# Performance work log

Measured on AMD Instinct MI355X. Metric: run time of the kernel, lower is better.

## Reference

```python
import jax, jax.numpy as jnp
import numpy as np

B, H, W, C = 8, 56, 56, 256
HEADS = 8      # block-level heads; each branch uses HEADS//2
SPLIT = 7      # split_size
EPS = 1e-5


def _ln(x, g, b):
    m = x.mean(-1, keepdims=True)
    v = ((x - m) ** 2).mean(-1, keepdims=True)
    return (x - m) * jax.lax.rsqrt(v + EPS) * g + b


def _lepe_attn(q, k, v, H_sp, W_sp, heads, cw, cb):
    # q,k,v: [B,H,W,Ch]; cross-shaped window attention with LePE depthwise conv bias
    Bq, Hq, Wq, Ch = q.shape
    hd = Ch // heads
    scale = hd ** -0.5
    nh, nw = Hq // H_sp, Wq // W_sp

    def win(t):  # -> [Bw, heads, L, hd]  (Bw = B*nh*nw, L = H_sp*W_sp)
        t = t.reshape(Bq, nh, H_sp, nw, W_sp, Ch).transpose(0, 1, 3, 2, 4, 5)
        return t.reshape(-1, H_sp * W_sp, heads, hd).transpose(0, 2, 1, 3)

    qw, kw = win(q), win(k)
    # v windows laid out NCHW for the depthwise LePE conv
    vimg = v.reshape(Bq, nh, H_sp, nw, W_sp, Ch).transpose(0, 1, 3, 5, 2, 4).reshape(-1, Ch, H_sp, W_sp)
    lepe = jax.lax.conv_general_dilated(
        vimg, cw, window_strides=(1, 1), padding=((1, 1), (1, 1)),
        feature_group_count=Ch, dimension_numbers=("NCHW", "OIHW", "NCHW"))
    lepe = lepe + cb[None, :, None, None]
    lepe = lepe.reshape(-1, heads, hd, H_sp * W_sp).transpose(0, 1, 3, 2)
    vw = vimg.reshape(-1, heads, hd, H_sp * W_sp).transpose(0, 1, 3, 2)

    attn = jax.nn.softmax(jnp.einsum("whld,whmd->whlm", qw * scale, kw), axis=-1)
    out = jnp.einsum("whlm,whmd->whld", attn, vw) + lepe  # [Bw,heads,L,hd]
    out = out.transpose(0, 2, 1, 3).reshape(-1, H_sp, W_sp, Ch)
    # windows2img
    out = out.reshape(Bq, nh, nw, H_sp, W_sp, Ch).transpose(0, 1, 3, 2, 4, 5).reshape(Bq, Hq, Wq, Ch)
    return out


def setup_inputs() -> dict:
    key = jax.random.key(0)
    ks = jax.random.split(key, 8)
    ch = C // 2
    s = 0.02
    return {
        "x": jax.random.normal(ks[0], (B, H, W, C), jnp.float32),
        "gamma1": jnp.ones((C,), jnp.float32), "beta1": jnp.zeros((C,), jnp.float32),
        "w_qkv": jax.random.normal(ks[1], (C, 3 * C), jnp.float32) * s,
        "lepe_w0": jax.random.normal(ks[2], (ch, 1, 3, 3), jnp.float32) * s,
        "lepe_b0": jnp.zeros((ch,), jnp.float32),
        "lepe_w1": jax.random.normal(ks[3], (ch, 1, 3, 3), jnp.float32) * s,
        "lepe_b1": jnp.zeros((ch,), jnp.float32),
        "w_proj": jax.random.normal(ks[4], (C, C), jnp.float32) * s,
        "b_proj": jnp.zeros((C,), jnp.float32),
        "gamma2": jnp.ones((C,), jnp.float32), "beta2": jnp.zeros((C,), jnp.float32),
        "w_fc1": jax.random.normal(ks[5], (C, 4 * C), jnp.float32) * s,
        "b_fc1": jnp.zeros((4 * C,), jnp.float32),
        "w_fc2": jax.random.normal(ks[6], (4 * C, C), jnp.float32) * s,
        "b_fc2": jnp.zeros((C,), jnp.float32),
    }


def reference(x, gamma1, beta1, w_qkv, lepe_w0, lepe_b0, lepe_w1, lepe_b1,
              w_proj, b_proj, gamma2, beta2, w_fc1, b_fc1, w_fc2, b_fc2):
    Bx, Hx, Wx, Cx = x.shape
    img = _ln(x, gamma1, beta1)
    qkv = (img @ w_qkv).reshape(Bx, Hx, Wx, 3, Cx).transpose(3, 0, 1, 2, 4)
    q, k, v = qkv[0], qkv[1], qkv[2]
    ch = Cx // 2
    heads = HEADS // 2
    # branch 0 (idx=0): H_sp=H, W_sp=split  -> vertical stripes
    x0 = _lepe_attn(q[..., :ch], k[..., :ch], v[..., :ch], Hx, SPLIT, heads, lepe_w0, lepe_b0)
    # branch 1 (idx=1): H_sp=split, W_sp=W  -> horizontal stripes
    x1 = _lepe_attn(q[..., ch:], k[..., ch:], v[..., ch:], SPLIT, Wx, heads, lepe_w1, lepe_b1)
    att = jnp.concatenate([x0, x1], axis=-1) @ w_proj + b_proj
    x = x + att
    h = _ln(x, gamma2, beta2)
    h = jax.nn.gelu(h @ w_fc1 + b_fc1, approximate=False) @ w_fc2 + b_fc2
    return x + h
```

## Files before the change

kernel.cpp:

```cpp
#include <hip/hip_runtime.h>
#include <stdint.h>

typedef __attribute__((ext_vector_type(4))) float  f32x4;
typedef __attribute__((ext_vector_type(8))) __bf16 bf16x8;

#define DEVI static __device__ __forceinline__

DEVI float bf2f_lo(uint32_t u) { union { uint32_t i; float f; } v; v.i = u << 16;          return v.f; }
DEVI float bf2f_hi(uint32_t u) { union { uint32_t i; float f; } v; v.i = u & 0xffff0000u;  return v.f; }
DEVI uint16_t f2bf(float f) {
    union { float f; uint32_t i; } v; v.f = f;
    uint32_t r = v.i + 0x7fffu + ((v.i >> 16) & 1u);
    return (uint16_t)(r >> 16);
}
DEVI void unpack8(uint4 u, float* f) {
    f[0] = bf2f_lo(u.x); f[1] = bf2f_hi(u.x);
    f[2] = bf2f_lo(u.y); f[3] = bf2f_hi(u.y);
    f[4] = bf2f_lo(u.z); f[5] = bf2f_hi(u.z);
    f[6] = bf2f_lo(u.w); f[7] = bf2f_hi(u.w);
}
DEVI void gload_lds16(const uint16_t* gp, uint16_t* lp) {
    __builtin_amdgcn_global_load_lds(
        (const __attribute__((address_space(1))) uint32_t*)gp,
        (__attribute__((address_space(3))) uint32_t*)lp, 16, 0, 0);
}

__global__ __launch_bounds__(256) void wprep(const float* __restrict__ w,
                                             uint16_t* __restrict__ wt, int K, int N) {
    int idx = blockIdx.x * 256 + threadIdx.x;
    if (idx >= K * N) return;
    int k = idx / N, n = idx - k * N;
    wt[(size_t)n * K + k] = f2bf(w[idx]);
}

__global__ __launch_bounds__(256) void ln_kernel(const float* __restrict__ x,
                                                 const float* __restrict__ g,
                                                 const float* __restrict__ be,
                                                 uint16_t* __restrict__ y) {
    int row  = blockIdx.x * 4 + (threadIdx.x >> 6);
    int lane = threadIdx.x & 63;
    const float* xr = x + (size_t)row * 256 + lane * 4;
    f32x4 v = *(const f32x4*)xr;
    float s  = v[0] + v[1] + v[2] + v[3];
    float s2 = v[0]*v[0] + v[1]*v[1] + v[2]*v[2] + v[3]*v[3];
#pragma unroll
    for (int off = 32; off > 0; off >>= 1) {
        s  += __shfl_xor(s, off);
        s2 += __shfl_xor(s2, off);
    }
    float mean = s * (1.f / 256.f);
    float var  = s2 * (1.f / 256.f) - mean * mean;
    float rs   = rsqrtf(var + 1e-5f);
    f32x4 gv = *(const f32x4*)(g  + lane * 4);
    f32x4 bv = *(const f32x4*)(be + lane * 4);
    uint64_t pk = 0;
#pragma unroll
    for (int j = 0; j < 4; ++j) {
        uint64_t b = f2bf((v[j] - mean) * rs * gv[j] + bv[j]);
        pk |= b << (16 * j);
    }
    *(uint64_t*)(y + (size_t)row * 256 + lane * 4) = pk;
}

template <int EPI>
__global__ __launch_bounds__(256) void gemm_bt(const uint16_t* __restrict__ A,
                                               const uint16_t* __restrict__ Bt,
                                               int M, int N, int K,
                                               const float* __restrict__ bias,
                                               const float* __restrict__ resid,
                                               void* __restrict__ outp) {
    __shared__ __align__(16) uint16_t As[2][128 * 32];
    __shared__ __align__(16) uint16_t Bs[2][128 * 32];
    const int tid  = threadIdx.x;
    const int lane = tid & 63;
    const int w    = tid >> 6;
    const int wr   = w >> 1, wc = w & 1;
    const int bm = blockIdx.x, bn = blockIdx.y;
    f32x4 acc[4][4] = {};
    const int nk = K >> 5;
    const int wb = w * 512;

    const int srow = tid >> 2;
    const int hwr  = (srow ^ (srow >> 2)) & 3;
    const size_t ao0 = (size_t)srow * K + (size_t)(((tid & 3) ^ hwr) * 8);
    const size_t ao1 = ao0 + (size_t)64 * K;

    const uint16_t* Abase = A  + (size_t)bm * 128 * K;
    const uint16_t* Bbase = Bt + (size_t)bn * 128 * K;

    auto stage = [&](int buf, int kk) {
        const uint16_t* Ab = Abase + kk * 32;
        const uint16_t* Bb = Bbase + kk * 32;
        gload_lds16(Ab + ao0, &As[buf][wb]);
        gload_lds16(Ab + ao1, &As[buf][wb + 2048]);
        gload_lds16(Bb + ao0, &Bs[buf][wb]);
        gload_lds16(Bb + ao1, &Bs[buf][wb + 2048]);
    };

    stage(0, 0);
    __syncthreads();
    int cur = 0;

    const int li = lane & 15;
    const int rA = wr * 64 + li;
    const int rB = wc * 64 + li;
    const int kx = ((lane >> 4) ^ ((li ^ (li >> 2)) & 3)) * 8;

    for (int kk = 0; kk < nk; ++kk) {
        if (kk + 1 < nk) stage(cur ^ 1, kk + 1);

        bf16x8 af[4], bfr[4];
#pragma unroll
        for (int m = 0; m < 4; ++m)
            af[m] = __builtin_bit_cast(bf16x8,
                     *(const uint4*)&As[cur][(rA + m * 16) * 32 + kx]);
#pragma unroll
        for (int n = 0; n < 4; ++n)
            bfr[n] = __builtin_bit_cast(bf16x8,
                      *(const uint4*)&Bs[cur][(rB + n * 16) * 32 + kx]);
#pragma unroll
        for (int m = 0; m < 4; ++m)
#pragma unroll
            for (int n = 0; n < 4; ++n)
                acc[m][n] = __builtin_amdgcn_mfma_f32_16x16x32_bf16(af[m], bfr[n], acc[m][n], 0, 0, 0);

        __syncthreads();
        cur ^= 1;
    }

    const int row0 = bm * 128 + wr * 64 + ((lane >> 4) * 4);
    const int col0 = bn * 128 + wc * 64 + li;
#pragma unroll
    for (int m = 0; m < 4; ++m) {
#pragma unroll
        for (int n = 0; n < 4; ++n) {
            const int col = col0 + n * 16;
#pragma unroll
            for (int r = 0; r < 4; ++r) {
                const int row = row0 + m * 16 + r;
                float v = acc[m][n][r];
                size_t idx = (size_t)row * N + col;
                if (EPI == 0) {
                    ((uint16_t*)outp)[idx] = f2bf(v);
                } else if (EPI == 1) {
                    ((float*)outp)[idx] = v + bias[col] + resid[idx];
                } else {
                    v += bias[col];
                    float ge = 0.5f * v * (1.0f + erff(v * 0.70710678118654752f));
                    ((uint16_t*)outp)[idx] = f2bf(ge);
                }
            }
        }
    }
}

__global__ __launch_bounds__(64) void attn_mfma(const uint16_t* __restrict__ qkv,
                                                uint16_t* __restrict__ att) {
    __shared__ __align__(16) uint16_t Pl[64 * 40];
    int bid = blockIdx.x;
    const int qtile = bid % 7;  bid /= 7;
    const int head  = bid & 3;  bid >>= 2;
    const int win   = bid & 63; bid >>= 6;
    const int branch = bid;
    const int lane = threadIdx.x;
    const int g  = lane >> 4;
    const int li = lane & 15;
    const int b = win >> 3, wp = win & 7;
    const int ch0 = branch * 128 + head * 32;
    const int base0 = b * 3136;
    const int woff  = wp * 7;
    const int toks1 = base0 + wp * 392;

    auto tokof = [&](int l) -> int {
        if (branch == 0) { int r = l / 7; return base0 + r * 56 + woff + (l - r * 7); }
        return toks1 + l;
    };
    const int tok391 = tokof(391);
    const int q0 = qtile * 64;

    bf16x8 qf[4];
#pragma unroll
    for (int nb = 0; nb < 4; ++nb) {
        int ql = q0 + nb * 16 + li; if (ql > 391) ql = 391;
        qf[nb] = __builtin_bit_cast(bf16x8,
                 *(const uint4*)(qkv + (size_t)tokof(ql) * 768 + ch0 + g * 8));
    }

    float m_run[4], s_run[4];
    f32x4 oacc[2][4];
#pragma unroll
    for (int nb = 0; nb < 4; ++nb) {
        m_run[nb] = -1e30f; s_run[nb] = 0.f;
        oacc[0][nb] = (f32x4)0.f; oacc[1][nb] = (f32x4)0.f;
    }
    const float scale = 0.17677669529663687f;

    for (int kt = 0; kt < 13; ++kt) {
        const int kbase = kt * 32;
        bf16x8 kf[2];
#pragma unroll
        for (int mb = 0; mb < 2; ++mb) {
            int kl = kbase + mb * 16 + li; if (kl > 391) kl = 391;
            kf[mb] = __builtin_bit_cast(bf16x8,
                     *(const uint4*)(qkv + (size_t)tokof(kl) * 768 + 256 + ch0 + g * 8));
        }
        uint16_t vg0[8], vg1[8];
        {
            int kl0 = kbase + g * 8;
            int tk, cc = 0;
            if (branch == 0) { int r = kl0 / 7; cc = kl0 - r * 7; tk = base0 + r * 56 + woff + cc; }
            else tk = toks1 + kl0;
#pragma unroll
            for (int j = 0; j < 8; ++j) {
                int t = (kl0 + j > 391) ? tok391 : tk;
                const uint16_t* vp = qkv + (size_t)t * 768 + 512 + ch0 + li;
                vg0[j] = vp[0];
                vg1[j] = vp[16];
                if (branch == 0) { if (++cc == 7) { cc = 0; tk += 50; } else ++tk; }
                else ++tk;
            }
        }
        f32x4 sa[2][4] = {};
#pragma unroll
        for (int mb = 0; mb < 2; ++mb)
#pragma unroll
            for (int nb = 0; nb < 4; ++nb)
                sa[mb][nb] = __builtin_amdgcn_mfma_f32_16x16x32_bf16(kf[mb], qf[nb], sa[mb][nb], 0, 0, 0);
#pragma unroll
        for (int mb = 0; mb < 2; ++mb)
#pragma unroll
            for (int nb = 0; nb < 4; ++nb)
#pragma unroll
                for (int r = 0; r < 4; ++r) sa[mb][nb][r] *= scale;
        if (kt == 12) {
#pragma unroll
            for (int nb = 0; nb < 4; ++nb)
#pragma unroll
                for (int r = 0; r < 4; ++r) {
                    if (g >= 2) sa[0][nb][r] = -1e30f;
                    sa[1][nb][r] = -1e30f;
                }
        }
#pragma unroll
        for (int nb = 0; nb < 4; ++nb) {
            f32x4 mx = sa[0][nb];
#pragma unroll
            for (int r = 0; r < 4; ++r) mx[r] = fmaxf(mx[r], sa[1][nb][r]);
            float mt = fmaxf(fmaxf(mx[0], mx[1]), fmaxf(mx[2], mx[3]));
            mt = fmaxf(mt, __shfl_xor(mt, 16));
            mt = fmaxf(mt, __shfl_xor(mt, 32));
            float m_new = fmaxf(m_run[nb], mt);
            float corr = __expf(m_run[nb] - m_new);
            m_run[nb] = m_new;
#pragma unroll
            for (int mb = 0; mb < 2; ++mb)
#pragma unroll
                for (int r = 0; r < 4; ++r) oacc[mb][nb][r] *= corr;
            float psum = 0.f;
            uint32_t pk[4];
#pragma unroll
            for (int mb = 0; mb < 2; ++mb) {
                float p0 = __expf(sa[mb][nb][0] - m_new);
                float p1 = __expf(sa[mb][nb][1] - m_new);
                float p2 = __expf(sa[mb][nb][2] - m_new);
                float p3 = __expf(sa[mb][nb][3] - m_new);
                psum += (p0 + p1) + (p2 + p3);
                pk[mb * 2 + 0] = (uint32_t)f2bf(p0) | ((uint32_t)f2bf(p1) << 16);
                pk[mb * 2 + 1] = (uint32_t)f2bf(p2) | ((uint32_t)f2bf(p3) << 16);
            }
            psum += __shfl_xor(psum, 16);
            psum += __shfl_xor(psum, 32);
            s_run[nb] = s_run[nb] * corr + psum;
            uint32_t* dst = (uint32_t*)&Pl[(li + 16 * nb) * 40];
            dst[g * 2 + 0] = pk[0];
            dst[g * 2 + 1] = pk[1];
            dst[g * 2 + 8] = pk[2];
            dst[g * 2 + 9] = pk[3];
        }
        union { uint16_t u[8]; bf16x8 v; } cv0, cv1;
#pragma unroll
        for (int j = 0; j < 8; ++j) { cv0.u[j] = vg0[j]; cv1.u[j] = vg1[j]; }
        bf16x8 vf0 = cv0.v, vf1 = cv1.v;
        bf16x8 pf[4];
#pragma unroll
        for (int nb = 0; nb < 4; ++nb)
            pf[nb] = __builtin_bit_cast(bf16x8,
                     *(const uint4*)&Pl[(li + 16 * nb) * 40 + g * 8]);
#pragma unroll
        for (int nb = 0; nb < 4; ++nb) {
            oacc[0][nb] = __builtin_amdgcn_mfma_f32_16x16x32_bf16(vf0, pf[nb], oacc[0][nb], 0, 0, 0);
            oacc[1][nb] = __builtin_amdgcn_mfma_f32_16x16x32_bf16(vf1, pf[nb], oacc[1][nb], 0, 0, 0);
        }
    }
#pragma unroll
    for (int nb = 0; nb < 4; ++nb) {
        int ql = q0 + nb * 16 + li;
        if (ql <= 391) {
            float rn = 1.f / s_run[nb];
            uint16_t* op = att + (size_t)tokof(ql) * 256 + ch0;
#pragma unroll
            for (int mb = 0; mb < 2; ++mb)
#pragma unroll
                for (int r = 0; r < 4; ++r)
                    op[mb * 16 + g * 4 + r] = f2bf(oacc[mb][nb][r] * rn);
        }
    }
}

__global__ __launch_bounds__(256) void lepe_kernel(const uint16_t* __restrict__ qkv,
                                                   const float* __restrict__ lw0,
                                                   const float* __restrict__ lb0,
                                                   const float* __restrict__ lw1,
                                                   const float* __restrict__ lb1,
                                                   uint16_t* __restrict__ att) {
    __shared__ float wl[9][256];
    __shared__ float bl[256];
    {
        int tid = threadIdx.x;
        for (int i = tid; i < 2304; i += 256) {
            int tap = i >> 8, ch = i & 255;
            wl[tap][ch] = (ch < 128) ? lw0[ch * 9 + tap] : lw1[(ch - 128) * 9 + tap];
        }
        bl[tid] = (tid < 128) ? lb0[tid] : lb1[tid - 128];
    }
    __syncthreads();

    int idx = blockIdx.x * 256 + threadIdx.x;
    int t = idx >> 5, cg = idx & 31;
    int ch = cg * 8;
    int branch = ch >> 7;
    int b = t / 3136, rem = t - b * 3136, h = rem / 56, w = rem - h * 56;
    int r0, r1, c0, c1;
    if (branch == 0) { r0 = 0; r1 = 55; int wp = w / 7; c0 = wp * 7; c1 = c0 + 6; }
    else             { int hp = h / 7; r0 = hp * 7; r1 = r0 + 6; c0 = 0; c1 = 55; }

    const uint16_t* vbase = qkv + (size_t)b * 3136 * 768 + 512 + ch;
    float acc[8];
    {
        f32x4 b0 = *(const f32x4*)&bl[ch];
        f32x4 b1 = *(const f32x4*)&bl[ch + 4];
#pragma unroll
        for (int d = 0; d < 4; ++d) { acc[d] = b0[d]; acc[d + 4] = b1[d]; }
    }
#pragma unroll
    for (int dy = -1; dy <= 1; ++dy) {
#pragma unroll
        for (int dx = -1; dx <= 1; ++dx) {
            int hh = h + dy, ww = w + dx;
            float mask = (hh >= r0 && hh <= r1 && ww >= c0 && ww <= c1) ? 1.f : 0.f;
            int hc = min(max(hh, r0), r1), wc = min(max(ww, c0), c1);
            uint4 u = *(const uint4*)(vbase + (size_t)(hc * 56 + wc) * 768);
            float vv[8]; unpack8(u, vv);
            const int tap = (dy + 1) * 3 + (dx + 1);
            f32x4 w0 = *(const f32x4*)&wl[tap][ch];
            f32x4 w1 = *(const f32x4*)&wl[tap][ch + 4];
#pragma unroll
            for (int d = 0; d < 4; ++d) {
                acc[d]     += (mask * w0[d]) * vv[d];
                acc[d + 4] += (mask * w1[d]) * vv[d + 4];
            }
        }
    }
    uint16_t* ap = att + (size_t)t * 256 + ch;
    uint4 a = *(const uint4*)ap;
    float av[8]; unpack8(a, av);
    uint16_t ob[8];
#pragma unroll
    for (int d = 0; d < 8; ++d) ob[d] = f2bf(av[d] + acc[d]);
    *(uint4*)ap = *(const uint4*)ob;
}

extern "C" void kernel_launch(void* const* d_in, const int* in_sizes, int n_in,
                              void* d_out, int out_size, void* d_ws, size_t ws_size,
                              hipStream_t stream) {
    const float* x      = (const float*)d_in[0];
    const float* g1     = (const float*)d_in[1];
    const float* be1    = (const float*)d_in[2];
    const float* w_qkv  = (const float*)d_in[3];
    const float* lw0    = (const float*)d_in[4];
    const float* lb0    = (const float*)d_in[5];
    const float* lw1    = (const float*)d_in[6];
    const float* lb1    = (const float*)d_in[7];
    const float* w_proj = (const float*)d_in[8];
    const float* b_proj = (const float*)d_in[9];
    const float* g2     = (const float*)d_in[10];
    const float* be2    = (const float*)d_in[11];
    const float* w_fc1  = (const float*)d_in[12];
    const float* b_fc1  = (const float*)d_in[13];
    const float* w_fc2  = (const float*)d_in[14];
    const float* b_fc2  = (const float*)d_in[15];
    float* out = (float*)d_out;

    char* p = (char*)d_ws;
    auto carve = [&](size_t bytes) -> char* {
        char* q = p; p += (bytes + 255) & ~(size_t)255; return q;
    };
    uint16_t* lnb    = (uint16_t*)carve((size_t)25088 * 256 * 2);
    uint16_t* qkvh   = (uint16_t*)carve((size_t)25088 * 1024 * 2);
    uint16_t* attb   = (uint16_t*)carve((size_t)25088 * 256 * 2);
    float*    x1     = (float*)   carve((size_t)25088 * 256 * 4);
    uint16_t* wqkvT  = (uint16_t*)carve((size_t)768 * 256 * 2);
    uint16_t* wprojT = (uint16_t*)carve((size_t)256 * 256 * 2);
    uint16_t* wfc1T  = (uint16_t*)carve((size_t)1024 * 256 * 2);
    uint16_t* wfc2T  = (uint16_t*)carve((size_t)256 * 1024 * 2);

    wprep<<<768,  256, 0, stream>>>(w_qkv,  wqkvT,  256, 768);
    wprep<<<256,  256, 0, stream>>>(w_proj, wprojT, 256, 256);
    wprep<<<1024, 256, 0, stream>>>(w_fc1,  wfc1T,  256, 1024);
    wprep<<<1024, 256, 0, stream>>>(w_fc2,  wfc2T,  1024, 256);

    ln_kernel<<<6272, 256, 0, stream>>>(x, g1, be1, lnb);
    gemm_bt<0><<<dim3(196, 6), 256, 0, stream>>>(lnb, wqkvT, 25088, 768, 256,
                                                 nullptr, nullptr, qkvh);
    attn_mfma<<<3584, 64, 0, stream>>>(qkvh, attb);
    lepe_kernel<<<3136, 256, 0, stream>>>(qkvh, lw0, lb0, lw1, lb1, attb);
    gemm_bt<1><<<dim3(196, 2), 256, 0, stream>>>(attb, wprojT, 25088, 256, 256,
                                                 b_proj, x, x1);
    ln_kernel<<<6272, 256, 0, stream>>>(x1, g2, be2, lnb);
    gemm_bt<2><<<dim3(196, 8), 256, 0, stream>>>(lnb, wfc1T, 25088, 1024, 256,
                                                 b_fc1, nullptr, qkvh);
    gemm_bt<1><<<dim3(196, 2), 256, 0, stream>>>(qkvh, wfc2T, 25088, 256, 1024,
                                                 b_fc2, x1, out);
}
```

Baseline: 310.2 us.

## Fold softmax scale into exp2, add lazy rescale, remap block order

The explicit multiply of the score tiles by the softmax scale is removed. The scale and log2(e) are folded into one constant used with exp2f and an fma. The running-max rescale of the accumulators now happens only when some lane's new max exceeds the old one by more than a threshold, which skips most of the correction multiplies. Block indices are permuted so that neighbouring workgroups land on different XCDs with a different grouping of window, head and tile, and the bf16 conversion uses the native cast. The lazy rescale lets exponentials grow up to 2^8 before correction, which is safe in fp32 but could in principle affect bf16 P precision.

```diff
diff --git a/kernel.cpp b/kernel.cpp
--- a/kernel.cpp
+++ b/kernel.cpp
@@ -157,11 +157,13 @@
 __global__ __launch_bounds__(64) void attn_mfma(const uint16_t* __restrict__ qkv,
                                                 uint16_t* __restrict__ att) {
     __shared__ __align__(16) uint16_t Pl[64 * 40];
-    int bid = blockIdx.x;
-    const int qtile = bid % 7;  bid /= 7;
-    const int head  = bid & 3;  bid >>= 2;
-    const int win   = bid & 63; bid >>= 6;
-    const int branch = bid;
+    int bid = ((int)blockIdx.x & 7) * 448 + ((int)blockIdx.x >> 3);
+    const int sub   = bid % 28;
+    const int winl  = bid / 28;
+    const int qtile = sub % 7;
+    const int head  = sub / 7;
+    const int win   = winl & 63;
+    const int branch = winl >> 6;
     const int lane = threadIdx.x;
     const int g  = lane >> 4;
     const int li = lane & 15;
@@ -193,7 +195,8 @@
         m_run[nb] = -1e30f; s_run[nb] = 0.f;
         oacc[0][nb] = (f32x4)0.f; oacc[1][nb] = (f32x4)0.f;
     }
-    const float scale = 0.17677669529663687f;
+    const float c = 0.25503486f;
+    const float THR = 31.368f;
 
     for (int kt = 0; kt < 13; ++kt) {
         const int kbase = kt * 32;
@@ -226,12 +229,6 @@
 #pragma unroll
             for (int nb = 0; nb < 4; ++nb)
                 sa[mb][nb] = __builtin_amdgcn_mfma_f32_16x16x32_bf16(kf[mb], qf[nb], sa[mb][nb], 0, 0, 0);
-#pragma unroll
-        for (int mb = 0; mb < 2; ++mb)
-#pragma unroll
-            for (int nb = 0; nb < 4; ++nb)
-#pragma unroll
-                for (int r = 0; r < 4; ++r) sa[mb][nb][r] *= scale;
         if (kt == 12) {
 #pragma unroll
             for (int nb = 0; nb < 4; ++nb)
@@ -243,34 +240,39 @@
         }
 #pragma unroll
         for (int nb = 0; nb < 4; ++nb) {
-            f32x4 mx = sa[0][nb];
-#pragma unroll
-            for (int r = 0; r < 4; ++r) mx[r] = fmaxf(mx[r], sa[1][nb][r]);
-            float mt = fmaxf(fmaxf(mx[0], mx[1]), fmaxf(mx[2], mx[3]));
+            float mt = fmaxf(fmaxf(fmaxf(sa[0][nb][0], sa[0][nb][1]), fmaxf(sa[0][nb][2], sa[0][nb][3])),
+                             fmaxf(fmaxf(sa[1][nb][0], sa[1][nb][1]), fmaxf(sa[1][nb][2], sa[1][nb][3])));
             mt = fmaxf(mt, __shfl_xor(mt, 16));
             mt = fmaxf(mt, __shfl_xor(mt, 32));
-            float m_new = fmaxf(m_run[nb], mt);
-            float corr = __expf(m_run[nb] - m_new);
-            m_run[nb] = m_new;
-#pragma unroll
-            for (int mb = 0; mb < 2; ++mb)
-#pragma unroll
-                for (int r = 0; r < 4; ++r) oacc[mb][nb][r] *= corr;
+            if (!__all(mt <= m_run[nb] + THR)) {
+                float m_new = fmaxf(m_run[nb], mt);
+                float corr = exp2f((m_run[nb] - m_new) * c);
+                m_run[nb] = m_new;
+                s_run[nb] *= corr;
+#pragma unroll
+                for (int mb = 0; mb < 2; ++mb)
+#pragma unroll
+                    for (int r = 0; r < 4; ++r) oacc[mb][nb][r] *= corr;
+            }
+            const float m2 = m_run[nb] * c;
             float psum = 0.f;
             uint32_t pk[4];
 #pragma unroll
             for (int mb = 0; mb < 2; ++mb) {
-                float p0 = __expf(sa[mb][nb][0] - m_new);
-                float p1 = __expf(sa[mb][nb][1] - m_new);
-                float p2 = __expf(sa[mb][nb][2] - m_new);
-                float p3 = __expf(sa[mb][nb][3] - m_new);
+                float p0 = exp2f(fmaf(sa[mb][nb][0], c, -m2));
+                float p1 = exp2f(fmaf(sa[mb][nb][1], c, -m2));
+                float p2 = exp2f(fmaf(sa[mb][nb][2], c, -m2));
+                float p3 = exp2f(fmaf(sa[mb][nb][3], c, -m2));
                 psum += (p0 + p1) + (p2 + p3);
-                pk[mb * 2 + 0] = (uint32_t)f2bf(p0) | ((uint32_t)f2bf(p1) << 16);
-                pk[mb * 2 + 1] = (uint32_t)f2bf(p2) | ((uint32_t)f2bf(p3) << 16);
+                union { __bf16 h[2]; uint32_t u; } ca, cb;
+                ca.h[0] = (__bf16)p0; ca.h[1] = (__bf16)p1;
+                cb.h[0] = (__bf16)p2; cb.h[1] = (__bf16)p3;
+                pk[mb * 2 + 0] = ca.u;
+                pk[mb * 2 + 1] = cb.u;
             }
             psum += __shfl_xor(psum, 16);
             psum += __shfl_xor(psum, 32);
-            s_run[nb] = s_run[nb] * corr + psum;
+            s_run[nb] += psum;
             uint32_t* dst = (uint32_t*)&Pl[(li + 16 * nb) * 40];
             dst[g * 2 + 0] = pk[0];
             dst[g * 2 + 1] = pk[1];
```

Result: no change. 310.9 us (+0.2%).
